# Kernel tuning notes

Hardware: AMD Instinct MI355X
Metric: run time of the kernel (lower is better)

## Reference

```python
import jax, jax.numpy as jnp
import numpy as np

B, L, D, H, DK, DV = 16, 1024, 512, 8, 64, 64
FACTOR = 1
TOP_K = int(FACTOR * np.log(L))  # 6, static


def autocorrelation(q, k, v, top_k):
    # q, k, v: [B, L, H, E] (Autoformer layout)
    Bs, Ls, Hs, Es = q.shape
    qp = jnp.transpose(q, (0, 2, 3, 1))  # [B,H,E,L]
    kp = jnp.transpose(k, (0, 2, 3, 1))
    vp = jnp.transpose(v, (0, 2, 3, 1))
    qf = jnp.fft.rfft(qp, axis=-1)
    kf = jnp.fft.rfft(kp, axis=-1)
    corr = jnp.fft.irfft(qf * jnp.conj(kf), n=Ls, axis=-1)  # [B,H,E,L]
    # time_delay_agg_training: average corr over heads and channels
    mean_value = corr.mean(axis=(1, 2))  # [B,L]
    _, index = jax.lax.top_k(mean_value.mean(axis=0), top_k)  # [top_k] shared delays
    weights = jnp.take(mean_value, index, axis=1)  # [B,top_k]
    tmp_corr = jax.nn.softmax(weights, axis=-1)  # [B,top_k]
    # roll(v, -delay) gathered for all top_k delays at once
    idx = (index[:, None] + jnp.arange(Ls)[None, :]) % Ls  # [top_k, L]
    patterns = vp[..., idx]  # [B,H,E,top_k,L]
    agg = jnp.einsum('bhekl,bk->bhel', patterns, tmp_corr)  # [B,H,E,L]
    return jnp.transpose(agg, (0, 3, 1, 2))  # [B,L,H,E]


def setup_inputs() -> dict:
    key = jax.random.key(0)
    ks = jax.random.split(key, 7)
    Q = jax.random.normal(ks[0], (B, L, D), jnp.float32)
    K = jax.random.normal(ks[1], (B, L, D), jnp.float32)
    V = jax.random.normal(ks[2], (B, L, D), jnp.float32)
    attn_mask = jnp.zeros((B, 1, L, L), jnp.bool_)  # ignored by AutoCorrelation
    s = 0.02
    WQ = jax.random.normal(ks[3], (D, H * DK), jnp.float32) * s
    WK = jax.random.normal(ks[4], (D, H * DK), jnp.float32) * s
    WV = jax.random.normal(ks[5], (D, H * DV), jnp.float32) * s
    Wfc = jax.random.normal(ks[6], (H * DV, D), jnp.float32) * s
    return {"Q": Q, "K": K, "V": V, "attn_mask": attn_mask,
            "WQ": WQ, "WK": WK, "WV": WV, "Wfc": Wfc}


def reference(Q, K, V, attn_mask, WQ, WK, WV, Wfc):
    del attn_mask  # full AutoCorrelation ignores the mask
    q_s = (Q @ WQ).reshape(B, L, H, DK)  # [B,L,H,dk]
    k_s = (K @ WK).reshape(B, L, H, DK)
    v_s = (V @ WV).reshape(B, L, H, DV)
    out = autocorrelation(q_s, k_s, v_s, TOP_K)  # [B,L,H,dv]
    context = out.reshape(B, L, H * DV)
    return context @ Wfc  # [B,L,D]
```

## Files before the change

kernel.cpp:

```cpp
#include <hip/hip_runtime.h>
#include <math.h>

namespace {

constexpr int Bb = 16;
constexpr int Ll = 1024;
constexpr int Dd = 512;
constexpr int TOPK = 6;

typedef short  short8 __attribute__((ext_vector_type(8)));
typedef float  f32x4  __attribute__((ext_vector_type(4)));

__device__ __forceinline__ short f2bf(float x) {
  unsigned u = __builtin_bit_cast(unsigned, x);
  u += 0x7fffu + ((u >> 16) & 1u);
  return (short)(u >> 16);
}
__device__ __forceinline__ float bf2f(short b) {
  unsigned u = ((unsigned)(unsigned short)b) << 16;
  return __builtin_bit_cast(float, u);
}
__device__ __forceinline__ void g2l16(const void* g, void* l) {
  __builtin_amdgcn_global_load_lds(
      (const __attribute__((address_space(1))) unsigned*)g,
      (__attribute__((address_space(3))) unsigned*)l, 16, 0, 0);
}
__device__ __forceinline__ short8 cvt8(float4 a, float4 b) {
  short8 o;
  o[0] = f2bf(a.x); o[1] = f2bf(a.y); o[2] = f2bf(a.z); o[3] = f2bf(a.w);
  o[4] = f2bf(b.x); o[5] = f2bf(b.y); o[6] = f2bf(b.z); o[7] = f2bf(b.w);
  return o;
}

__global__ __launch_bounds__(256) void proj_gemm(
    const float* __restrict__ Qf, const float* __restrict__ Kf,
    const float* __restrict__ Vf,
    const short* __restrict__ wq, const short* __restrict__ wk,
    const short* __restrict__ wv,
    short* __restrict__ oq, short* __restrict__ ok, short* __restrict__ ov)
{
  constexpr int N = 512, K = 512;
  __shared__ short As[2][4096];
  __shared__ short Bs[2][4096];

  const int z = blockIdx.z;
  const float* Af = (z == 0) ? Qf : (z == 1) ? Kf : Vf;
  const short* Bp = (z == 0) ? wq : (z == 1) ? wk : wv;
  short*       C  = (z == 0) ? oq : (z == 1) ? ok : ov;

  const int f  = blockIdx.x + 4 * blockIdx.y;
  const int s  = (f & 7) * 64 + (f >> 3);
  const int n0 = (s & 3) * 128;
  const int m0 = (s >> 2) * 128;

  const int tid  = threadIdx.x;
  const int srow = tid >> 2;
  const int scol = (tid & 3) * 8;
  const float* fa0 = Af + (size_t)(m0 + srow) * K + scol;
  const float* fa1 = fa0 + (size_t)64 * K;
  const short* gb0 = Bp + (size_t)(n0 + srow) * K + scol;
  const short* gb1 = gb0 + (size_t)64 * K;

  const int lane = tid & 63;
  const int wave = tid >> 6;
  const int wr = wave >> 1, wc = wave & 1;
  const int lo = lane & 15, hi = lane >> 4;

  f32x4 acc[4][4];
#pragma unroll
  for (int i = 0; i < 4; ++i)
#pragma unroll
    for (int j = 0; j < 4; ++j) acc[i][j] = (f32x4){0.f, 0.f, 0.f, 0.f};

  float4 ra0, ra1, ra2, ra3;
#define AISSUE(k) do { \
    ra0 = *(const float4*)(fa0 + (k));     ra1 = *(const float4*)(fa0 + (k) + 4); \
    ra2 = *(const float4*)(fa1 + (k));     ra3 = *(const float4*)(fa1 + (k) + 4); } while (0)
#define AWRITE(buf) do { \
    *(short8*)&As[buf][tid * 8]        = cvt8(ra0, ra1); \
    *(short8*)&As[buf][2048 + tid * 8] = cvt8(ra2, ra3); } while (0)
#define BISSUE(buf, k) do { \
    g2l16(gb0 + (k), &Bs[buf][tid * 8]); \
    g2l16(gb1 + (k), &Bs[buf][2048 + tid * 8]); } while (0)

  AISSUE(0); BISSUE(0, 0); AWRITE(0);
  __syncthreads();

  int cur = 0;
  for (int k0 = 0; k0 < K; k0 += 32) {
    const bool more = (k0 + 32 < K);
    if (more) { AISSUE(k0 + 32); BISSUE(cur ^ 1, k0 + 32); }
    short8 af[4], bfr[4];
#pragma unroll
    for (int i = 0; i < 4; ++i)
      af[i] = *(const short8*)&As[cur][(wr * 64 + i * 16 + lo) * 32 + hi * 8];
#pragma unroll
    for (int j = 0; j < 4; ++j)
      bfr[j] = *(const short8*)&Bs[cur][(wc * 64 + j * 16 + lo) * 32 + hi * 8];
#pragma unroll
    for (int i = 0; i < 4; ++i)
#pragma unroll
      for (int j = 0; j < 4; ++j)
        acc[i][j] = __builtin_amdgcn_mfma_f32_16x16x32_bf16(af[i], bfr[j], acc[i][j], 0, 0, 0);
    if (more) AWRITE(cur ^ 1);
    __syncthreads();
    cur ^= 1;
  }
#undef AISSUE
#undef AWRITE
#undef BISSUE

#pragma unroll
  for (int i = 0; i < 4; ++i)
#pragma unroll
    for (int r = 0; r < 4; ++r) {
      const size_t row = m0 + wr * 64 + i * 16 + hi * 4 + r;
#pragma unroll
      for (int j = 0; j < 4; ++j)
        C[row * N + n0 + wc * 64 + j * 16 + lo] = f2bf(acc[i][j][r]);
    }
}

__global__ __launch_bounds__(256) void corr_gemm(
    const short* __restrict__ A, const short* __restrict__ BT,
    float* __restrict__ mv)
{
  constexpr int K = 512;
  __shared__ short As[2][4096];
  __shared__ short Bs[2][4096];
  __shared__ float bins[256];

  const int bz = blockIdx.z;
  const int f  = blockIdx.x + 8 * blockIdx.y;
  const int s  = (f & 7) * 8 + (f >> 3);
  const int n0 = (s & 7) * 128;
  const int m0 = (s >> 3) * 128;
  const short* Ab = A  + (size_t)bz * Ll * K;
  const short* Bp = BT + (size_t)bz * Ll * K;

  const int tid  = threadIdx.x;
  const int srow = tid >> 2;
  const int scol = (tid & 3) * 8;
  const short* ga0 = Ab + (size_t)(m0 + srow) * K + scol;
  const short* ga1 = ga0 + (size_t)64 * K;
  const short* gb0 = Bp + (size_t)(n0 + srow) * K + scol;
  const short* gb1 = gb0 + (size_t)64 * K;

  const int lane = tid & 63;
  const int wave = tid >> 6;
  const int wr = wave >> 1, wc = wave & 1;
  const int lo = lane & 15, hi = lane >> 4;

  bins[tid] = 0.f;

  f32x4 acc[4][4];
#pragma unroll
  for (int i = 0; i < 4; ++i)
#pragma unroll
    for (int j = 0; j < 4; ++j) acc[i][j] = (f32x4){0.f, 0.f, 0.f, 0.f};

#define STAGE(buf, k) do { \
    g2l16(ga0 + (k), &As[buf][tid * 8]); \
    g2l16(ga1 + (k), &As[buf][2048 + tid * 8]); \
    g2l16(gb0 + (k), &Bs[buf][tid * 8]); \
    g2l16(gb1 + (k), &Bs[buf][2048 + tid * 8]); } while (0)

  STAGE(0, 0);
  __syncthreads();

  int cur = 0;
  for (int k0 = 0; k0 < K; k0 += 32) {
    if (k0 + 32 < K) STAGE(cur ^ 1, k0 + 32);
    short8 af[4], bfr[4];
#pragma unroll
    for (int i = 0; i < 4; ++i)
      af[i] = *(const short8*)&As[cur][(wr * 64 + i * 16 + lo) * 32 + hi * 8];
#pragma unroll
    for (int j = 0; j < 4; ++j)
      bfr[j] = *(const short8*)&Bs[cur][(wc * 64 + j * 16 + lo) * 32 + hi * 8];
#pragma unroll
    for (int i = 0; i < 4; ++i)
#pragma unroll
      for (int j = 0; j < 4; ++j)
        acc[i][j] = __builtin_amdgcn_mfma_f32_16x16x32_bf16(af[i], bfr[j], acc[i][j], 0, 0, 0);
    __syncthreads();
    cur ^= 1;
  }
#undef STAGE

  float red[7][4];
#pragma unroll
  for (int d = 0; d < 7; ++d)
#pragma unroll
    for (int r = 0; r < 4; ++r) red[d][r] = 0.f;
#pragma unroll
  for (int i = 0; i < 4; ++i)
#pragma unroll
    for (int j = 0; j < 4; ++j)
#pragma unroll
      for (int r = 0; r < 4; ++r) red[i - j + 3][r] += acc[i][j][r];

  const int dbase = 127 + (wr - wc) * 64 + 4 * hi - lo;
#pragma unroll
  for (int d = 0; d < 7; ++d)
#pragma unroll
    for (int r = 0; r < 4; ++r)
      atomicAdd(&bins[dbase + 16 * (d - 3) + r], red[d][r]);
  __syncthreads();
  if (tid < 255) {
    const int l = (m0 - n0 + tid - 127) & (Ll - 1);
    atomicAdd(&mv[bz * Ll + l], bins[tid]);
  }
}

__global__ __launch_bounds__(256) void fc_gemm(
    const short* __restrict__ A, const short* __restrict__ BT,
    float* __restrict__ C)
{
  constexpr int N = 512, K = 512;
  __shared__ short As[2][4096];
  __shared__ short Bs[2][4096];

  const int f  = blockIdx.x + 4 * blockIdx.y;
  const int s  = (f & 7) * 64 + (f >> 3);
  const int n0 = (s & 3) * 128;
  const int m0 = (s >> 2) * 128;

  const int tid  = threadIdx.x;
  const int srow = tid >> 2;
  const int scol = (tid & 3) * 8;
  const short* ga0 = A + (size_t)(m0 + srow) * K + scol;
  const short* ga1 = ga0 + (size_t)64 * K;
  const short* gb0 = BT + (size_t)(n0 + srow) * K + scol;
  const short* gb1 = gb0 + (size_t)64 * K;

  const int lane = tid & 63;
  const int wave = tid >> 6;
  const int wr = wave >> 1, wc = wave & 1;
  const int lo = lane & 15, hi = lane >> 4;

  f32x4 acc[4][4];
#pragma unroll
  for (int i = 0; i < 4; ++i)
#pragma unroll
    for (int j = 0; j < 4; ++j) acc[i][j] = (f32x4){0.f, 0.f, 0.f, 0.f};

#define STAGE(buf, k) do { \
    g2l16(ga0 + (k), &As[buf][tid * 8]); \
    g2l16(ga1 + (k), &As[buf][2048 + tid * 8]); \
    g2l16(gb0 + (k), &Bs[buf][tid * 8]); \
    g2l16(gb1 + (k), &Bs[buf][2048 + tid * 8]); } while (0)

  STAGE(0, 0);
  __syncthreads();

  int cur = 0;
  for (int k0 = 0; k0 < K; k0 += 32) {
    if (k0 + 32 < K) STAGE(cur ^ 1, k0 + 32);
    short8 af[4], bfr[4];
#pragma unroll
    for (int i = 0; i < 4; ++i)
      af[i] = *(const short8*)&As[cur][(wr * 64 + i * 16 + lo) * 32 + hi * 8];
#pragma unroll
    for (int j = 0; j < 4; ++j)
      bfr[j] = *(const short8*)&Bs[cur][(wc * 64 + j * 16 + lo) * 32 + hi * 8];
#pragma unroll
    for (int i = 0; i < 4; ++i)
#pragma unroll
      for (int j = 0; j < 4; ++j)
        acc[i][j] = __builtin_amdgcn_mfma_f32_16x16x32_bf16(af[i], bfr[j], acc[i][j], 0, 0, 0);
    __syncthreads();
    cur ^= 1;
  }
#undef STAGE

#pragma unroll
  for (int i = 0; i < 4; ++i)
#pragma unroll
    for (int r = 0; r < 4; ++r) {
      const size_t row = m0 + wr * 64 + i * 16 + hi * 4 + r;
#pragma unroll
      for (int j = 0; j < 4; ++j)
        C[row * N + n0 + wc * 64 + j * 16 + lo] = acc[i][j][r];
    }
}

__global__ __launch_bounds__(256) void wtrans(
    const float* __restrict__ w0, const float* __restrict__ w1,
    const float* __restrict__ w2, const float* __restrict__ w3,
    short* __restrict__ o0, short* __restrict__ o1,
    short* __restrict__ o2, short* __restrict__ o3)
{
  const int z = blockIdx.z;
  const float* W = (z == 0) ? w0 : (z == 1) ? w1 : (z == 2) ? w2 : w3;
  short* O = (z == 0) ? o0 : (z == 1) ? o1 : (z == 2) ? o2 : o3;
  __shared__ float t[32][33];
  const int tx = threadIdx.x & 31, ty = threadIdx.x >> 5;
  const int bx = blockIdx.x, by = blockIdx.y;
#pragma unroll
  for (int s = 0; s < 32; s += 8)
    t[ty + s][tx] = W[(size_t)(by * 32 + ty + s) * 512 + bx * 32 + tx];
  __syncthreads();
#pragma unroll
  for (int s = 0; s < 32; s += 8)
    O[(size_t)(bx * 32 + ty + s) * 512 + by * 32 + tx] = f2bf(t[tx][ty + s]);
}

__global__ void zero_mv(float* __restrict__ mv)
{
  int i = blockIdx.x * 256 + threadIdx.x;
  if (i < Bb * Ll) mv[i] = 0.f;
}

__global__ __launch_bounds__(1024) void topk_softmax(
    const float* __restrict__ mean_value,
    int* __restrict__ idx_out, float* __restrict__ w_out)
{
  __shared__ float vals[1024];
  __shared__ int   inds[1024];
  __shared__ float bm[1024];
  __shared__ int   topi[TOPK];
  const int t = threadIdx.x;
  float s = 0.f;
  for (int b = 0; b < Bb; ++b) s += mean_value[b * Ll + t];
  bm[t] = s;
  __syncthreads();
  for (int k = 0; k < TOPK; ++k) {
    bool taken = false;
    for (int j = 0; j < k; ++j) taken |= (topi[j] == t);
    vals[t] = taken ? -INFINITY : bm[t];
    inds[t] = t;
    __syncthreads();
    for (int stride = 512; stride > 0; stride >>= 1) {
      if (t < stride) {
        if (vals[t + stride] > vals[t]) { vals[t] = vals[t + stride]; inds[t] = inds[t + stride]; }
      }
      __syncthreads();
    }
    if (t == 0) topi[k] = inds[0];
    __syncthreads();
  }
  if (t < TOPK) idx_out[t] = topi[t];
  if (t < Bb) {
    float wv[TOPK], mx = -INFINITY;
#pragma unroll
    for (int k = 0; k < TOPK; ++k) {
      wv[k] = mean_value[t * Ll + topi[k]] * (1.f / 512.f);
      mx = fmaxf(mx, wv[k]);
    }
    float sum = 0.f;
#pragma unroll
    for (int k = 0; k < TOPK; ++k) { wv[k] = expf(wv[k] - mx); sum += wv[k]; }
#pragma unroll
    for (int k = 0; k < TOPK; ++k) w_out[t * TOPK + k] = wv[k] / sum;
  }
}

__global__ __launch_bounds__(256) void aggregate(
    const short* __restrict__ vs, const float* __restrict__ w,
    const int* __restrict__ idx, short* __restrict__ ctx)
{
  const int b = blockIdx.y;
  __shared__ float ww[8];
  __shared__ int   ii[8];
  if (threadIdx.x < TOPK) { ww[threadIdx.x] = w[b * TOPK + threadIdx.x]; ii[threadIdx.x] = idx[threadIdx.x]; }
  __syncthreads();
  const int l = blockIdx.x * 4 + (threadIdx.x >> 6);
  const int c = (threadIdx.x & 63) * 8;
  const short* vb = vs + (size_t)b * Ll * Dd;
  float a[8] = {};
#pragma unroll
  for (int k = 0; k < TOPK; ++k) {
    const short8 vv = *(const short8*)&vb[(size_t)((l + ii[k]) & (Ll - 1)) * Dd + c];
    const float wk = ww[k];
#pragma unroll
    for (int e = 0; e < 8; ++e) a[e] = fmaf(wk, bf2f(vv[e]), a[e]);
  }
  short8 o;
#pragma unroll
  for (int e = 0; e < 8; ++e) o[e] = f2bf(a[e]);
  *(short8*)&ctx[((size_t)b * Ll + l) * Dd + c] = o;
}

}

extern "C" void kernel_launch(void* const* d_in, const int* in_sizes, int n_in,
                              void* d_out, int out_size, void* d_ws, size_t ws_size,
                              hipStream_t stream)
{
  const float* Q   = (const float*)d_in[0];
  const float* K   = (const float*)d_in[1];
  const float* V   = (const float*)d_in[2];
  const float* WQ  = (const float*)d_in[4];
  const float* WK  = (const float*)d_in[5];
  const float* WV  = (const float*)d_in[6];
  const float* Wfc = (const float*)d_in[7];
  float* out = (float*)d_out;

  char* ws = (char*)d_ws;
  const size_t SB = (size_t)Bb * Ll * Dd * sizeof(short);
  short* qsb  = (short*)(ws);
  short* ksb  = (short*)(ws + 1 * SB);
  short* vsb  = (short*)(ws + 2 * SB);
  short* ctxb = (short*)(ws + 3 * SB);
  short* wtq  = (short*)(ws + 4 * SB);
  short* wtk  = wtq + 512 * 512;
  short* wtv  = wtk + 512 * 512;
  short* wtf  = wtv + 512 * 512;
  float* mv   = (float*)(wtf + 512 * 512);
  float* w    = mv + Bb * Ll;
  int*   idx  = (int*)(w + 128);

  wtrans<<<dim3(16, 16, 4), 256, 0, stream>>>(WQ, WK, WV, Wfc, wtq, wtk, wtv, wtf);
  zero_mv<<<64, 256, 0, stream>>>(mv);

  proj_gemm<<<dim3(4, 128, 3), 256, 0, stream>>>(Q, K, V, wtq, wtk, wtv, qsb, ksb, vsb);
  corr_gemm<<<dim3(8, 8, 16), 256, 0, stream>>>(qsb, ksb, mv);
  topk_softmax<<<1, 1024, 0, stream>>>(mv, idx, w);
  aggregate<<<dim3(Ll / 4, Bb), 256, 0, stream>>>(vsb, w, idx, ctxb);
  fc_gemm<<<dim3(4, 128, 1), 256, 0, stream>>>(ctxb, wtf, out);
}
```

Measured before the change: 160.6 us.

## Enlarge GEMM tiles with bigger workgroups, swizzled LDS, and fused zeroing

Reworks the three GEMM kernels to use larger workgroups and tiles. The projection GEMM now covers 128x512 per 1024-thread block, so each float A row is read and converted once instead of four times. The correlation GEMM uses 256x256 tiles and the fc GEMM 128x256. LDS layouts get an XOR swizzle to avoid bank conflicts, the projection output is staged through LDS for 16-byte coalesced stores, and the mv zeroing is folded into the weight-transpose kernel to save a launch. Fewer, larger blocks cut redundant global loads, at the risk of lower occupancy and poorer wave-count balance across CUs.

```diff
diff --git a/kernel.cpp b/kernel.cpp
--- a/kernel.cpp
+++ b/kernel.cpp
@@ -7,7 +7,9 @@
 constexpr int Ll = 1024;
 constexpr int Dd = 512;
 constexpr int TOPK = 6;
-
+constexpr int Kc = 512;
+
+typedef short  short4v __attribute__((ext_vector_type(4)));
 typedef short  short8 __attribute__((ext_vector_type(8)));
 typedef float  f32x4  __attribute__((ext_vector_type(4)));
 
@@ -32,39 +34,50 @@
   return o;
 }
 
-__global__ __launch_bounds__(256) void proj_gemm(
+__global__ __launch_bounds__(1024) void proj_gemm(
     const float* __restrict__ Qf, const float* __restrict__ Kf,
     const float* __restrict__ Vf,
     const short* __restrict__ wq, const short* __restrict__ wk,
     const short* __restrict__ wv,
     short* __restrict__ oq, short* __restrict__ ok, short* __restrict__ ov)
 {
-  constexpr int N = 512, K = 512;
-  __shared__ short As[2][4096];
-  __shared__ short Bs[2][4096];
-
-  const int z = blockIdx.z;
+  __shared__ short lds[2][20480];
+
+  const int tid = threadIdx.x;
+  const int fb = blockIdx.x;
+  const int s  = (fb & 7) * 48 + (fb >> 3);
+  const int z  = s / 128;
+  const int m0 = (s % 128) * 128;
+
   const float* Af = (z == 0) ? Qf : (z == 1) ? Kf : Vf;
   const short* Bp = (z == 0) ? wq : (z == 1) ? wk : wv;
   short*       C  = (z == 0) ? oq : (z == 1) ? ok : ov;
 
-  const int f  = blockIdx.x + 4 * blockIdx.y;
-  const int s  = (f & 7) * 64 + (f >> 3);
-  const int n0 = (s & 3) * 128;
-  const int m0 = (s >> 2) * 128;
-
-  const int tid  = threadIdx.x;
-  const int srow = tid >> 2;
-  const int scol = (tid & 3) * 8;
-  const float* fa0 = Af + (size_t)(m0 + srow) * K + scol;
-  const float* fa1 = fa0 + (size_t)64 * K;
-  const short* gb0 = Bp + (size_t)(n0 + srow) * K + scol;
-  const short* gb1 = gb0 + (size_t)64 * K;
+  const int rowA = tid >> 3, qA = tid & 7;
+  const float* gA = Af + (size_t)(m0 + rowA) * Kc + qA * 4;
+  const int offA = (rowA * 4 + ((qA >> 1) ^ ((rowA >> 1) & 3))) * 8 + (qA & 1) * 4;
+
+  const int rB0 = tid >> 2,           c80 = (tid & 3) ^ ((rB0 >> 1) & 3);
+  const int rB1 = (1024 + tid) >> 2,  c81 = (tid & 3) ^ ((rB1 >> 1) & 3);
+  const short* gB0 = Bp + (size_t)rB0 * Kc + c80 * 8;
+  const short* gB1 = Bp + (size_t)rB1 * Kc + c81 * 8;
+  const int dB0 = 4096 + tid * 8, dB1 = 4096 + (1024 + tid) * 8;
 
   const int lane = tid & 63;
-  const int wave = tid >> 6;
-  const int wr = wave >> 1, wc = wave & 1;
+  const int wid  = tid >> 6;
+  const int wm = wid >> 3, wn = wid & 7;
   const int lo = lane & 15, hi = lane >> 4;
+  int aoff[4], boff[4];
+#pragma unroll
+  for (int i = 0; i < 4; ++i) {
+    const int ar = wm * 64 + i * 16 + lo;
+    aoff[i] = (ar * 4 + (hi ^ ((ar >> 1) & 3))) * 8;
+  }
+#pragma unroll
+  for (int j = 0; j < 4; ++j) {
+    const int br = wn * 64 + j * 16 + lo;
+    boff[j] = 4096 + (br * 4 + (hi ^ ((br >> 1) & 3))) * 8;
+  }
 
   f32x4 acc[4][4];
 #pragma unroll
@@ -72,86 +85,106 @@
 #pragma unroll
     for (int j = 0; j < 4; ++j) acc[i][j] = (f32x4){0.f, 0.f, 0.f, 0.f};
 
-  float4 ra0, ra1, ra2, ra3;
-#define AISSUE(k) do { \
-    ra0 = *(const float4*)(fa0 + (k));     ra1 = *(const float4*)(fa0 + (k) + 4); \
-    ra2 = *(const float4*)(fa1 + (k));     ra3 = *(const float4*)(fa1 + (k) + 4); } while (0)
-#define AWRITE(buf) do { \
-    *(short8*)&As[buf][tid * 8]        = cvt8(ra0, ra1); \
-    *(short8*)&As[buf][2048 + tid * 8] = cvt8(ra2, ra3); } while (0)
-#define BISSUE(buf, k) do { \
-    g2l16(gb0 + (k), &Bs[buf][tid * 8]); \
-    g2l16(gb1 + (k), &Bs[buf][2048 + tid * 8]); } while (0)
-
-  AISSUE(0); BISSUE(0, 0); AWRITE(0);
-  __syncthreads();
-
-  int cur = 0;
-  for (int k0 = 0; k0 < K; k0 += 32) {
-    const bool more = (k0 + 32 < K);
-    if (more) { AISSUE(k0 + 32); BISSUE(cur ^ 1, k0 + 32); }
+  {
+    const float4 v = *(const float4*)(gA);
+    g2l16(gB0, &lds[0][dB0]);
+    g2l16(gB1, &lds[0][dB1]);
+    short4v s4; s4[0] = f2bf(v.x); s4[1] = f2bf(v.y); s4[2] = f2bf(v.z); s4[3] = f2bf(v.w);
+    *(short4v*)&lds[0][offA] = s4;
+  }
+  __syncthreads();
+
+#pragma unroll 1
+  for (int t = 0; t < 16; ++t) {
+    const int cur = t & 1;
+    const short* L = &lds[cur][0];
     short8 af[4], bfr[4];
 #pragma unroll
-    for (int i = 0; i < 4; ++i)
-      af[i] = *(const short8*)&As[cur][(wr * 64 + i * 16 + lo) * 32 + hi * 8];
-#pragma unroll
-    for (int j = 0; j < 4; ++j)
-      bfr[j] = *(const short8*)&Bs[cur][(wc * 64 + j * 16 + lo) * 32 + hi * 8];
+    for (int i = 0; i < 4; ++i) af[i]  = *(const short8*)(L + aoff[i]);
+#pragma unroll
+    for (int j = 0; j < 4; ++j) bfr[j] = *(const short8*)(L + boff[j]);
+
+    float4 av;
+    if (t < 15) {
+      const int ke = (t + 1) * 32;
+      av = *(const float4*)(gA + ke);
+      g2l16(gB0 + ke, &lds[cur ^ 1][dB0]);
+      g2l16(gB1 + ke, &lds[cur ^ 1][dB1]);
+    }
+
 #pragma unroll
     for (int i = 0; i < 4; ++i)
 #pragma unroll
       for (int j = 0; j < 4; ++j)
         acc[i][j] = __builtin_amdgcn_mfma_f32_16x16x32_bf16(af[i], bfr[j], acc[i][j], 0, 0, 0);
-    if (more) AWRITE(cur ^ 1);
-    __syncthreads();
-    cur ^= 1;
-  }
-#undef AISSUE
-#undef AWRITE
-#undef BISSUE
-
-#pragma unroll
-  for (int i = 0; i < 4; ++i)
-#pragma unroll
-    for (int r = 0; r < 4; ++r) {
-      const size_t row = m0 + wr * 64 + i * 16 + hi * 4 + r;
+
+    if (t < 15) {
+      short4v s4; s4[0] = f2bf(av.x); s4[1] = f2bf(av.y); s4[2] = f2bf(av.z); s4[3] = f2bf(av.w);
+      *(short4v*)&lds[cur ^ 1][offA] = s4;
+    }
+    __syncthreads();
+  }
+
+  short* eb = &lds[0][0];
+  const int wid2 = tid >> 6, rem = tid & 63;
+  const int rr = rem >> 2, c0 = (rem & 3) * 16;
+  const size_t orow = (size_t)(m0 + (wid2 >> 3) * 64) * Dd + (wid2 & 7) * 64 + c0;
+#pragma unroll
+  for (int i = 0; i < 4; ++i) {
+    if (i) __syncthreads();
+#pragma unroll
+    for (int r = 0; r < 4; ++r)
 #pragma unroll
       for (int j = 0; j < 4; ++j)
-        C[row * N + n0 + wc * 64 + j * 16 + lo] = f2bf(acc[i][j][r]);
-    }
-}
-
-__global__ __launch_bounds__(256) void corr_gemm(
+        eb[wid * 1088 + (hi * 4 + r) * 68 + j * 16 + lo] = f2bf(acc[i][j][r]);
+    __syncthreads();
+    const short8 v0 = *(const short8*)&eb[wid2 * 1088 + rr * 68 + c0];
+    const short8 v1 = *(const short8*)&eb[wid2 * 1088 + rr * 68 + c0 + 8];
+    *(short8*)&C[orow + (size_t)(i * 16 + rr) * Dd]     = v0;
+    *(short8*)&C[orow + (size_t)(i * 16 + rr) * Dd + 8] = v1;
+  }
+}
+
+__global__ __launch_bounds__(1024) void corr_gemm(
     const short* __restrict__ A, const short* __restrict__ BT,
     float* __restrict__ mv)
 {
-  constexpr int K = 512;
-  __shared__ short As[2][4096];
-  __shared__ short Bs[2][4096];
-  __shared__ float bins[256];
-
-  const int bz = blockIdx.z;
-  const int f  = blockIdx.x + 8 * blockIdx.y;
-  const int s  = (f & 7) * 8 + (f >> 3);
-  const int n0 = (s & 7) * 128;
-  const int m0 = (s >> 3) * 128;
-  const short* Ab = A  + (size_t)bz * Ll * K;
-  const short* Bp = BT + (size_t)bz * Ll * K;
-
-  const int tid  = threadIdx.x;
-  const int srow = tid >> 2;
-  const int scol = (tid & 3) * 8;
-  const short* ga0 = Ab + (size_t)(m0 + srow) * K + scol;
-  const short* ga1 = ga0 + (size_t)64 * K;
-  const short* gb0 = Bp + (size_t)(n0 + srow) * K + scol;
-  const short* gb1 = gb0 + (size_t)64 * K;
+  __shared__ short lds[2][16384];
+  __shared__ float bins[512];
+
+  const int tid = threadIdx.x;
+  const int fb = blockIdx.x;
+  const int s  = (fb & 7) * 32 + (fb >> 3);
+  const int z  = s >> 4;
+  const int m0 = ((s >> 2) & 3) * 256;
+  const int n0 = (s & 3) * 256;
+
+  const short* Ab = A  + (size_t)z * Ll * Kc;
+  const short* Bp = BT + (size_t)z * Ll * Kc;
+
+  const int rS  = tid >> 2;
+  const int c8S = (tid & 3) ^ ((rS >> 1) & 3);
+  const short* gA = Ab + (size_t)(m0 + rS) * Kc + c8S * 8;
+  const short* gB = Bp + (size_t)(n0 + rS) * Kc + c8S * 8;
+  const int dA = tid * 8, dB = 8192 + tid * 8;
 
   const int lane = tid & 63;
-  const int wave = tid >> 6;
-  const int wr = wave >> 1, wc = wave & 1;
+  const int wid  = tid >> 6;
+  const int wm = wid >> 2, wn = wid & 3;
   const int lo = lane & 15, hi = lane >> 4;
-
-  bins[tid] = 0.f;
+  int aoff[4], boff[4];
+#pragma unroll
+  for (int i = 0; i < 4; ++i) {
+    const int ar = wm * 64 + i * 16 + lo;
+    aoff[i] = (ar * 4 + (hi ^ ((ar >> 1) & 3))) * 8;
+  }
+#pragma unroll
+  for (int j = 0; j < 4; ++j) {
+    const int br = wn * 64 + j * 16 + lo;
+    boff[j] = 8192 + (br * 4 + (hi ^ ((br >> 1) & 3))) * 8;
+  }
+
+  if (tid < 512) bins[tid] = 0.f;
 
   f32x4 acc[4][4];
 #pragma unroll
@@ -159,34 +192,33 @@
 #pragma unroll
     for (int j = 0; j < 4; ++j) acc[i][j] = (f32x4){0.f, 0.f, 0.f, 0.f};
 
-#define STAGE(buf, k) do { \
-    g2l16(ga0 + (k), &As[buf][tid * 8]); \
-    g2l16(ga1 + (k), &As[buf][2048 + tid * 8]); \
-    g2l16(gb0 + (k), &Bs[buf][tid * 8]); \
-    g2l16(gb1 + (k), &Bs[buf][2048 + tid * 8]); } while (0)
-
-  STAGE(0, 0);
-  __syncthreads();
-
-  int cur = 0;
-  for (int k0 = 0; k0 < K; k0 += 32) {
-    if (k0 + 32 < K) STAGE(cur ^ 1, k0 + 32);
+  g2l16(gA, &lds[0][dA]);
+  g2l16(gB, &lds[0][dB]);
+  __syncthreads();
+
+#pragma unroll 1
+  for (int t = 0; t < 16; ++t) {
+    const int cur = t & 1;
+    const short* L = &lds[cur][0];
     short8 af[4], bfr[4];
 #pragma unroll
-    for (int i = 0; i < 4; ++i)
-      af[i] = *(const short8*)&As[cur][(wr * 64 + i * 16 + lo) * 32 + hi * 8];
-#pragma unroll
-    for (int j = 0; j < 4; ++j)
-      bfr[j] = *(const short8*)&Bs[cur][(wc * 64 + j * 16 + lo) * 32 + hi * 8];
+    for (int i = 0; i < 4; ++i) af[i]  = *(const short8*)(L + aoff[i]);
+#pragma unroll
+    for (int j = 0; j < 4; ++j) bfr[j] = *(const short8*)(L + boff[j]);
+
+    if (t < 15) {
+      const int ke = (t + 1) * 32;
+      g2l16(gA + ke, &lds[cur ^ 1][dA]);
+      g2l16(gB + ke, &lds[cur ^ 1][dB]);
+    }
+
 #pragma unroll
     for (int i = 0; i < 4; ++i)
 #pragma unroll
       for (int j = 0; j < 4; ++j)
         acc[i][j] = __builtin_amdgcn_mfma_f32_16x16x32_bf16(af[i], bfr[j], acc[i][j], 0, 0, 0);
     __syncthreads();
-    cur ^= 1;
-  }
-#undef STAGE
+  }
 
   float red[7][4];
 #pragma unroll
@@ -200,44 +232,56 @@
 #pragma unroll
       for (int r = 0; r < 4; ++r) red[i - j + 3][r] += acc[i][j][r];
 
-  const int dbase = 127 + (wr - wc) * 64 + 4 * hi - lo;
+  const int dbase = 255 + (wm - wn) * 64 + 4 * hi - lo;
 #pragma unroll
   for (int d = 0; d < 7; ++d)
 #pragma unroll
     for (int r = 0; r < 4; ++r)
       atomicAdd(&bins[dbase + 16 * (d - 3) + r], red[d][r]);
   __syncthreads();
-  if (tid < 255) {
-    const int l = (m0 - n0 + tid - 127) & (Ll - 1);
-    atomicAdd(&mv[bz * Ll + l], bins[tid]);
-  }
-}
-
-__global__ __launch_bounds__(256) void fc_gemm(
+  if (tid < 511) {
+    const int l = (m0 - n0 + tid - 255) & (Ll - 1);
+    atomicAdd(&mv[z * Ll + l], bins[tid]);
+  }
+}
+
+__global__ __launch_bounds__(512) void fc_gemm(
     const short* __restrict__ A, const short* __restrict__ BT,
     float* __restrict__ C)
 {
-  constexpr int N = 512, K = 512;
-  __shared__ short As[2][4096];
-  __shared__ short Bs[2][4096];
-
-  const int f  = blockIdx.x + 4 * blockIdx.y;
-  const int s  = (f & 7) * 64 + (f >> 3);
-  const int n0 = (s & 3) * 128;
-  const int m0 = (s >> 2) * 128;
-
-  const int tid  = threadIdx.x;
-  const int srow = tid >> 2;
-  const int scol = (tid & 3) * 8;
-  const short* ga0 = A + (size_t)(m0 + srow) * K + scol;
-  const short* ga1 = ga0 + (size_t)64 * K;
-  const short* gb0 = BT + (size_t)(n0 + srow) * K + scol;
-  const short* gb1 = gb0 + (size_t)64 * K;
+  __shared__ short lds[2][12288];
+
+  const int tid = threadIdx.x;
+  const int fb = blockIdx.x;
+  const int s  = (fb & 7) * 32 + (fb >> 3);
+  const int m0 = (s >> 1) * 128;
+  const int n0 = (s & 1) * 256;
+
+  const int rA  = tid >> 2;
+  const int c8A = (tid & 3) ^ ((rA >> 1) & 3);
+  const short* gA = A + (size_t)(m0 + rA) * Kc + c8A * 8;
+  const int dA = tid * 8;
+  const int rB0 = tid >> 2,          c8B0 = (tid & 3) ^ ((rB0 >> 1) & 3);
+  const int rB1 = (512 + tid) >> 2,  c8B1 = (tid & 3) ^ ((rB1 >> 1) & 3);
+  const short* gB0 = BT + (size_t)(n0 + rB0) * Kc + c8B0 * 8;
+  const short* gB1 = BT + (size_t)(n0 + rB1) * Kc + c8B1 * 8;
+  const int dB0 = 4096 + tid * 8, dB1 = 4096 + (512 + tid) * 8;
 
   const int lane = tid & 63;
-  const int wave = tid >> 6;
-  const int wr = wave >> 1, wc = wave & 1;
+  const int wid  = tid >> 6;
+  const int wm = wid >> 2, wn = wid & 3;
   const int lo = lane & 15, hi = lane >> 4;
+  int aoff[4], boff[4];
+#pragma unroll
+  for (int i = 0; i < 4; ++i) {
+    const int ar = wm * 64 + i * 16 + lo;
+    aoff[i] = (ar * 4 + (hi ^ ((ar >> 1) & 3))) * 8;
+  }
+#pragma unroll
+  for (int j = 0; j < 4; ++j) {
+    const int br = wn * 64 + j * 16 + lo;
+    boff[j] = 4096 + (br * 4 + (hi ^ ((br >> 1) & 3))) * 8;
+  }
 
   f32x4 acc[4][4];
 #pragma unroll
@@ -245,51 +289,53 @@
 #pragma unroll
     for (int j = 0; j < 4; ++j) acc[i][j] = (f32x4){0.f, 0.f, 0.f, 0.f};
 
-#define STAGE(buf, k) do { \
-    g2l16(ga0 + (k), &As[buf][tid * 8]); \
-    g2l16(ga1 + (k), &As[buf][2048 + tid * 8]); \
-    g2l16(gb0 + (k), &Bs[buf][tid * 8]); \
-    g2l16(gb1 + (k), &Bs[buf][2048 + tid * 8]); } while (0)
-
-  STAGE(0, 0);
-  __syncthreads();
-
-  int cur = 0;
-  for (int k0 = 0; k0 < K; k0 += 32) {
-    if (k0 + 32 < K) STAGE(cur ^ 1, k0 + 32);
+  g2l16(gA,  &lds[0][dA]);
+  g2l16(gB0, &lds[0][dB0]);
+  g2l16(gB1, &lds[0][dB1]);
+  __syncthreads();
+
+#pragma unroll 1
+  for (int t = 0; t < 16; ++t) {
+    const int cur = t & 1;
+    const short* L = &lds[cur][0];
     short8 af[4], bfr[4];
 #pragma unroll
-    for (int i = 0; i < 4; ++i)
-      af[i] = *(const short8*)&As[cur][(wr * 64 + i * 16 + lo) * 32 + hi * 8];
-#pragma unroll
-    for (int j = 0; j < 4; ++j)
-      bfr[j] = *(const short8*)&Bs[cur][(wc * 64 + j * 16 + lo) * 32 + hi * 8];
+    for (int i = 0; i < 4; ++i) af[i]  = *(const short8*)(L + aoff[i]);
+#pragma unroll
+    for (int j = 0; j < 4; ++j) bfr[j] = *(const short8*)(L + boff[j]);
+
+    if (t < 15) {
+      const int ke = (t + 1) * 32;
+      g2l16(gA  + ke, &lds[cur ^ 1][dA]);
+      g2l16(gB0 + ke, &lds[cur ^ 1][dB0]);
+      g2l16(gB1 + ke, &lds[cur ^ 1][dB1]);
+    }
+
 #pragma unroll
     for (int i = 0; i < 4; ++i)
 #pragma unroll
       for (int j = 0; j < 4; ++j)
         acc[i][j] = __builtin_amdgcn_mfma_f32_16x16x32_bf16(af[i], bfr[j], acc[i][j], 0, 0, 0);
     __syncthreads();
-    cur ^= 1;
-  }
-#undef STAGE
+  }
 
 #pragma unroll
   for (int i = 0; i < 4; ++i)
 #pragma unroll
     for (int r = 0; r < 4; ++r) {
-      const size_t row = m0 + wr * 64 + i * 16 + hi * 4 + r;
+      const size_t row = m0 + wm * 64 + i * 16 + hi * 4 + r;
 #pragma unroll
       for (int j = 0; j < 4; ++j)
-        C[row * N + n0 + wc * 64 + j * 16 + lo] = acc[i][j][r];
-    }
-}
-
-__global__ __launch_bounds__(256) void wtrans(
+        C[row * Dd + n0 + wn * 64 + j * 16 + lo] = acc[i][j][r];
+    }
+}
+
+__global__ __launch_bounds__(256) void prep(
     const float* __restrict__ w0, const float* __restrict__ w1,
     const float* __restrict__ w2, const float* __restrict__ w3,
     short* __restrict__ o0, short* __restrict__ o1,
-    short* __restrict__ o2, short* __restrict__ o3)
+    short* __restrict__ o2, short* __restrict__ o3,
+    float* __restrict__ mv)
 {
   const int z = blockIdx.z;
   const float* W = (z == 0) ? w0 : (z == 1) ? w1 : (z == 2) ? w2 : w3;
@@ -304,12 +350,10 @@
 #pragma unroll
   for (int s = 0; s < 32; s += 8)
     O[(size_t)(bx * 32 + ty + s) * 512 + by * 32 + tx] = f2bf(t[tx][ty + s]);
-}
-
-__global__ void zero_mv(float* __restrict__ mv)
-{
-  int i = blockIdx.x * 256 + threadIdx.x;
-  if (i < Bb * Ll) mv[i] = 0.f;
+  if (z == 0 && threadIdx.x < 64) {
+    const int fb = by * 16 + bx;
+    mv[fb * 64 + threadIdx.x] = 0.f;
+  }
 }
 
 __global__ __launch_bounds__(1024) void topk_softmax(
@@ -411,12 +455,14 @@
   float* w    = mv + Bb * Ll;
   int*   idx  = (int*)(w + 128);
 
-  wtrans<<<dim3(16, 16, 4), 256, 0, stream>>>(WQ, WK, WV, Wfc, wtq, wtk, wtv, wtf);
-  zero_mv<<<64, 256, 0, stream>>>(mv);
-
-  proj_gemm<<<dim3(4, 128, 3), 256, 0, stream>>>(Q, K, V, wtq, wtk, wtv, qsb, ksb, vsb);
-  corr_gemm<<<dim3(8, 8, 16), 256, 0, stream>>>(qsb, ksb, mv);
+  prep<<<dim3(16, 16, 4), 256, 0, stream>>>(WQ, WK, WV, Wfc, wtq, wtk, wtv, wtf, mv);
+
+  proj_gemm<<<dim3(384, 1, 1), 1024, 0, stream>>>(Q, K, V, wtq, wtk, wtv, qsb, ksb, vsb);
+
+  corr_gemm<<<dim3(256, 1, 1), 1024, 0, stream>>>(qsb, ksb, mv);
+
   topk_softmax<<<1, 1024, 0, stream>>>(mv, idx, w);
   aggregate<<<dim3(Ll / 4, Bb), 256, 0, stream>>>(vsb, w, idx, ctxb);
-  fc_gemm<<<dim3(4, 128, 1), 256, 0, stream>>>(ctxb, wtf, out);
-}
+
+  fc_gemm<<<dim3(256, 1, 1), 512, 0, stream>>>(ctxb, wtf, out);
+}
```

After: 158.8 us. Within noise of the previous version (-1.1%).
